# Optimization experiments

Hardware: AMD Instinct MI355X
Metric: run time of the kernel (lower is better)

The kernel has to match this reference:

```python
import jax, jax.numpy as jnp
import numpy as np

N_NODES = 20000
N_EDGES = 160000
N_GRAPHS = 64
IN_DIM = 128
HID = 512
N_CLASSES = 16


def setup_inputs() -> dict:
    key = jax.random.key(0)
    ks = jax.random.split(key, 16)
    x = jax.random.normal(ks[0], (N_NODES, IN_DIM), jnp.float32)
    src = jax.random.randint(ks[1], (N_EDGES,), 0, N_NODES, jnp.int32)
    dst = jax.random.randint(ks[2], (N_EDGES,), 0, N_NODES, jnp.int32)
    graph_ids = jnp.sort(jax.random.randint(ks[3], (N_NODES,), 0, N_GRAPHS, jnp.int32))

    def glorot(k, shape):
        lim = float(np.sqrt(6.0 / (shape[0] + shape[1])))
        return jax.random.uniform(k, shape, jnp.float32, -lim, lim)

    return {
        "x": x, "src": src, "dst": dst, "graph_ids": graph_ids,
        "W1": glorot(ks[4], (IN_DIM, HID)), "b1": jnp.zeros((HID,), jnp.float32),
        "W2": glorot(ks[5], (HID, HID)), "b2": jnp.zeros((HID,), jnp.float32),
        "W3": glorot(ks[6], (HID, HID)), "b3": jnp.zeros((HID,), jnp.float32),
        "Wc1": glorot(ks[7], (HID, HID)), "bc1": jnp.zeros((HID,), jnp.float32),
        "Wc2": glorot(ks[8], (HID, HID)), "bc2": jnp.zeros((HID,), jnp.float32),
        "Wc3": glorot(ks[9], (HID, N_CLASSES)), "bc3": jnp.zeros((N_CLASSES,), jnp.float32),
    }


def _graph_conv(h, W, b, src, dst, dout_isqrt, din_isqrt):
    # DGL GraphConv, norm='both': h' = D_in^{-1/2} A D_out^{-1/2} h W + b
    h = h * dout_isqrt[:, None]          # pre-normalize by sqrt(out-degree)
    h = h @ W                             # project first (cheaper than on edges)
    msg = h[src]                          # gather  [E, out]
    agg = jax.ops.segment_sum(msg, dst, num_segments=N_NODES)  # scatter-add
    return agg * din_isqrt[:, None] + b   # post-normalize by sqrt(in-degree)


def reference(x, src, dst, graph_ids, W1, b1, W2, b2, W3, b3,
              Wc1, bc1, Wc2, bc2, Wc3, bc3):
    ones_e = jnp.ones((N_EDGES,), jnp.float32)
    deg_out = jax.ops.segment_sum(ones_e, src, num_segments=N_NODES)
    deg_in = jax.ops.segment_sum(ones_e, dst, num_segments=N_NODES)
    dout_isqrt = jax.lax.rsqrt(jnp.clip(deg_out, 1.0))
    din_isqrt = jax.lax.rsqrt(jnp.clip(deg_in, 1.0))

    h = jax.nn.relu(_graph_conv(x, W1, b1, src, dst, dout_isqrt, din_isqrt))
    h = jax.nn.relu(_graph_conv(h, W2, b2, src, dst, dout_isqrt, din_isqrt))
    h = jax.nn.relu(_graph_conv(h, W3, b3, src, dst, dout_isqrt, din_isqrt))

    # dgl.mean_nodes: per-graph mean pooling
    sums = jax.ops.segment_sum(h, graph_ids, num_segments=N_GRAPHS)
    counts = jax.ops.segment_sum(jnp.ones((N_NODES,), jnp.float32), graph_ids,
                                 num_segments=N_GRAPHS)
    hg = sums / jnp.clip(counts, 1.0)[:, None]   # [G, HID]

    out = jax.nn.relu(hg @ Wc1 + bc1)
    out = jax.nn.relu(out @ Wc2 + bc2)
    return out @ Wc3 + bc3                       # [G, n_classes]
```

## Files before the change

### kernel.cpp

```cpp
#include <hip/hip_runtime.h>

#define N_NODES 20000
#define N_EDGES 160000
#define N_GRAPHS 64
#define IN_DIM 128
#define HID 512
#define N_CLASSES 16

#define POISON_I ((int)0xAAAAAAAA)

#define DEGCAP 40

typedef unsigned short u16;
typedef short bf16x8 __attribute__((ext_vector_type(8)));
typedef float f32x4 __attribute__((ext_vector_type(4)));

__device__ __forceinline__ u16 bf16_rn(float x) {
  unsigned u = __float_as_uint(x);
  unsigned r = u + 0x7FFFu + ((u >> 16) & 1u);
  return (u16)(r >> 16);
}

__device__ __forceinline__ void addh(float* a, int h) {
  a[0] += __uint_as_float((unsigned)h << 16);
  a[1] += __uint_as_float((unsigned)h & 0xFFFF0000u);
}

#define DEG_BLOCKS ((N_EDGES + 255) / 256)
__global__ void prep(const int* __restrict__ src, const int* __restrict__ dst,
                     int* __restrict__ dout, int* __restrict__ din,
                     int* __restrict__ cursor, int* __restrict__ bucket,
                     const float* __restrict__ W1, const float* __restrict__ W2,
                     const float* __restrict__ W3,
                     u16* __restrict__ w1h, u16* __restrict__ w2h,
                     u16* __restrict__ w3h) {
  if (blockIdx.x < DEG_BLOCKS) {
    const int e = blockIdx.x * 256 + threadIdx.x;
    if (e < N_EDGES) {
      const int s = src[e];
      const int d = dst[e];
      atomicAdd(dout + s, 1);
      atomicAdd(din + d, 1);
      const int pos = atomicAdd(cursor + d, 1) - POISON_I;
      if (pos < DEGCAP) bucket[d * DEGCAP + pos] = s;
    }
  } else {
    const int idx = (blockIdx.x - DEG_BLOCKS) * 256 + threadIdx.x;
    const int n1 = IN_DIM * HID;
    const int n2 = HID * HID;
    const float* W; u16* th; int K, N, j;
    if (idx < n1)             { W = W1; th = w1h; K = IN_DIM; N = HID; j = idx; }
    else if (idx < n1 + n2)   { W = W2; th = w2h; K = HID;    N = HID; j = idx - n1; }
    else if (idx < n1 + 2*n2) { W = W3; th = w3h; K = HID;    N = HID; j = idx - n1 - n2; }
    else return;
    const int k = j / N;
    const int n = j - k * N;
    th[(size_t)n * K + k] = bf16_rn(W[j]);
  }
}

__global__ __launch_bounds__(256) void norms(const int* __restrict__ dout,
                                             const int* __restrict__ din,
                                             float* __restrict__ dosq,
                                             float* __restrict__ disq,
                                             const int* __restrict__ gid,
                                             int* __restrict__ gstart) {
  const int i = blockIdx.x * 256 + threadIdx.x;
  if (i >= N_NODES) return;
  dosq[i] = rsqrtf(fmaxf((float)(dout[i] - POISON_I), 1.0f));
  disq[i] = rsqrtf(fmaxf((float)(din[i] - POISON_I), 1.0f));
  const int g = gid[i];
  const int gp = (i == 0) ? -1 : gid[i - 1];
  for (int k = gp + 1; k <= g; k++) gstart[k] = i;
  if (i == N_NODES - 1) {
    for (int k = g + 1; k <= N_GRAPHS; k++) gstart[k] = N_NODES;
  }
}

__global__ __launch_bounds__(256) void gather_f32(
    const float* __restrict__ x, const int* __restrict__ din,
    const int* __restrict__ bucket, const float* __restrict__ dosq,
    const float* __restrict__ disq, u16* __restrict__ gh) {
  const int node = blockIdx.x * 8 + (threadIdx.x >> 5);
  if (node >= N_NODES) return;
  const int lane4 = (threadIdx.x & 31) * 4;

  int cnt = din[node] - POISON_I;
  if (cnt > DEGCAP) cnt = DEGCAP;
  const int beg = node * DEGCAP;
  const int end = beg + cnt;

  float4 acc = make_float4(0.f, 0.f, 0.f, 0.f);
  int e = beg;
  for (; e + 4 <= end; e += 4) {
    const int s0 = bucket[e], s1 = bucket[e + 1], s2 = bucket[e + 2], s3 = bucket[e + 3];
    const float d0 = dosq[s0], d1 = dosq[s1], d2 = dosq[s2], d3 = dosq[s3];
    const float4 v0 = *(const float4*)(x + (size_t)s0 * IN_DIM + lane4);
    const float4 v1 = *(const float4*)(x + (size_t)s1 * IN_DIM + lane4);
    const float4 v2 = *(const float4*)(x + (size_t)s2 * IN_DIM + lane4);
    const float4 v3 = *(const float4*)(x + (size_t)s3 * IN_DIM + lane4);
    acc.x += d0 * v0.x + d1 * v1.x + d2 * v2.x + d3 * v3.x;
    acc.y += d0 * v0.y + d1 * v1.y + d2 * v2.y + d3 * v3.y;
    acc.z += d0 * v0.z + d1 * v1.z + d2 * v2.z + d3 * v3.z;
    acc.w += d0 * v0.w + d1 * v1.w + d2 * v2.w + d3 * v3.w;
  }
  for (; e < end; e++) {
    const int s0 = bucket[e];
    const float d0 = dosq[s0];
    const float4 v0 = *(const float4*)(x + (size_t)s0 * IN_DIM + lane4);
    acc.x += d0 * v0.x; acc.y += d0 * v0.y; acc.z += d0 * v0.z; acc.w += d0 * v0.w;
  }
  const float di = disq[node];
  ushort4 vh;
  vh.x = bf16_rn(acc.x * di);
  vh.y = bf16_rn(acc.y * di);
  vh.z = bf16_rn(acc.z * di);
  vh.w = bf16_rn(acc.w * di);
  *(ushort4*)(gh + (size_t)node * IN_DIM + lane4) = vh;
}

__global__ __launch_bounds__(256) void gather_hi(
    const u16* __restrict__ hin, const int* __restrict__ din,
    const int* __restrict__ bucket, const float* __restrict__ disq,
    u16* __restrict__ gh) {
  const int node = blockIdx.x * 4 + (threadIdx.x >> 6);
  if (node >= N_NODES) return;
  const int c8 = (threadIdx.x & 63) * 8;
  const u16* base = hin + c8;

  int cnt = din[node] - POISON_I;
  if (cnt > DEGCAP) cnt = DEGCAP;
  const int beg = node * DEGCAP;
  const int end = beg + cnt;

  float acc[8] = {};
  int e = beg;
  for (; e + 8 <= end; e += 8) {
    int s[8];
#pragma unroll
    for (int q = 0; q < 8; q++) s[q] = bucket[e + q];
    int4 h[8];
#pragma unroll
    for (int q = 0; q < 8; q++) h[q] = *(const int4*)(base + (size_t)s[q] * HID);
#pragma unroll
    for (int q = 0; q < 8; q++) {
      addh(acc + 0, h[q].x); addh(acc + 2, h[q].y);
      addh(acc + 4, h[q].z); addh(acc + 6, h[q].w);
    }
  }
  for (; e + 4 <= end; e += 4) {
    const int s0 = bucket[e], s1 = bucket[e + 1], s2 = bucket[e + 2], s3 = bucket[e + 3];
    const int4 h0 = *(const int4*)(base + (size_t)s0 * HID);
    const int4 h1 = *(const int4*)(base + (size_t)s1 * HID);
    const int4 h2 = *(const int4*)(base + (size_t)s2 * HID);
    const int4 h3 = *(const int4*)(base + (size_t)s3 * HID);
    addh(acc + 0, h0.x); addh(acc + 2, h0.y); addh(acc + 4, h0.z); addh(acc + 6, h0.w);
    addh(acc + 0, h1.x); addh(acc + 2, h1.y); addh(acc + 4, h1.z); addh(acc + 6, h1.w);
    addh(acc + 0, h2.x); addh(acc + 2, h2.y); addh(acc + 4, h2.z); addh(acc + 6, h2.w);
    addh(acc + 0, h3.x); addh(acc + 2, h3.y); addh(acc + 4, h3.z); addh(acc + 6, h3.w);
  }
  for (; e < end; e++) {
    const int4 h0 = *(const int4*)(base + (size_t)bucket[e] * HID);
    addh(acc + 0, h0.x); addh(acc + 2, h0.y); addh(acc + 4, h0.z); addh(acc + 6, h0.w);
  }

  const float di = disq[node];
  int4 hi;
  int* hp = (int*)&hi;
#pragma unroll
  for (int i = 0; i < 4; i++) {
    const u16 h0 = bf16_rn(acc[2 * i] * di);
    const u16 h1 = bf16_rn(acc[2 * i + 1] * di);
    hp[i] = (int)h0 | ((int)h1 << 16);
  }
  *(int4*)(gh + (size_t)node * HID + c8) = hi;
}

#define GBK 32
#define LROW 40
template <int POOL>
__global__ __launch_bounds__(256) void gemm_mfma(
    const u16* __restrict__ Ah, int lda,
    const u16* __restrict__ Bh,
    const float* __restrict__ bias, const float* __restrict__ dosq,
    u16* __restrict__ Cb,
    const int* __restrict__ gid, float* __restrict__ hgp,
    int M, int K) {
  __shared__ u16 sAh[128 * LROW];
  __shared__ u16 sBh[128 * LROW];

  const int n = blockIdx.x;
  const int r = (n & 7) + (n >> 5) * 8;
  const int c = (n >> 3) & 3;
  const int row0 = r * 128;
  const int col0 = c * 128;
  if (row0 >= M) return;

  const int t = threadIdx.x;
  const int lane = t & 63;
  const int wav  = t >> 6;
  const int wr = (wav >> 1) * 64;
  const int wc = (wav & 1) * 64;
  const int fm = lane & 15;
  const int fq = lane >> 4;

  const int r0 = t >> 2;
  const int u0 = t & 3;

  f32x4 acc[4][4] = {};

  for (int k0 = 0; k0 < K; k0 += GBK) {
    __syncthreads();
    int4 va[2], vc[2];
#pragma unroll
    for (int rep = 0; rep < 2; rep++) {
      const int row = r0 + rep * 64;
      const int arow = row0 + row;
      const bool ok = arow < M;
      const size_t aoff = (size_t)(ok ? arow : 0) * lda + k0 + u0 * 8;
      va[rep] = ok ? *(const int4*)(Ah + aoff) : make_int4(0, 0, 0, 0);
      const size_t boff = (size_t)(col0 + row) * K + k0 + u0 * 8;
      vc[rep] = *(const int4*)(Bh + boff);
    }
#pragma unroll
    for (int rep = 0; rep < 2; rep++) {
      const int ldso = (r0 + rep * 64) * LROW + u0 * 8;
      *(int4*)(sAh + ldso) = va[rep];
      *(int4*)(sBh + ldso) = vc[rep];
    }
    __syncthreads();

    bf16x8 fah[4], fbh[4];
#pragma unroll
    for (int i = 0; i < 4; i++) {
      const int ar = (wr + i * 16 + fm) * LROW + fq * 8;
      fah[i] = *(const bf16x8*)(sAh + ar);
      const int br = (wc + i * 16 + fm) * LROW + fq * 8;
      fbh[i] = *(const bf16x8*)(sBh + br);
    }
#pragma unroll
    for (int j = 0; j < 4; j++)
#pragma unroll
      for (int i = 0; i < 4; i++)
        acc[i][j] = __builtin_amdgcn_mfma_f32_16x16x32_bf16(fah[i], fbh[j], acc[i][j], 0, 0, 0);
  }

  if (POOL == 0) {
#pragma unroll
    for (int i = 0; i < 4; i++) {
#pragma unroll
      for (int rr = 0; rr < 4; rr++) {
        const int grow = row0 + wr + i * 16 + fq * 4 + rr;
        if (grow < M) {
          const float dsc = dosq[grow];
#pragma unroll
          for (int j = 0; j < 4; j++) {
            const int gcol = col0 + wc + j * 16 + fm;
            const float v = fmaxf(acc[i][j][rr] + bias[gcol], 0.0f) * dsc;
            Cb[(size_t)grow * HID + gcol] = bf16_rn(v);
          }
        }
      }
    }
  } else {
    __syncthreads();
    float* pool = (float*)sAh;
    const int g0 = gid[row0];
    const int rl = (row0 + 127 < M) ? row0 + 127 : M - 1;
    const int gspan = gid[rl] - g0 + 1;
    if (gspan <= 8) {
      for (int i = t; i < gspan * 128; i += 256) pool[i] = 0.f;
      __syncthreads();
#pragma unroll
      for (int j = 0; j < 4; j++) {
        const int lcol = wc + j * 16 + fm;
        const float bv = bias[col0 + lcol];
        float run = 0.f;
        int cur = -1;
#pragma unroll
        for (int i = 0; i < 4; i++)
#pragma unroll
          for (int rr = 0; rr < 4; rr++) {
            const int grow = row0 + wr + i * 16 + fq * 4 + rr;
            if (grow < M) {
              const int sg = gid[grow] - g0;
              const float v = fmaxf(acc[i][j][rr] + bv, 0.0f);
              if (sg != cur) {
                if (cur >= 0) atomicAdd(pool + cur * 128 + lcol, run);
                run = 0.f;
                cur = sg;
              }
              run += v;
            }
          }
        if (cur >= 0) atomicAdd(pool + cur * 128 + lcol, run);
      }
      __syncthreads();
      for (int i = t; i < gspan * 128; i += 256)
        atomicAdd(hgp + (size_t)(g0 + (i >> 7)) * HID + col0 + (i & 127), pool[i]);
    } else {
#pragma unroll
      for (int j = 0; j < 4; j++) {
        const int lcol = wc + j * 16 + fm;
        const float bv = bias[col0 + lcol];
        float run = 0.f;
        int cur = -1;
#pragma unroll
        for (int i = 0; i < 4; i++)
#pragma unroll
          for (int rr = 0; rr < 4; rr++) {
            const int grow = row0 + wr + i * 16 + fq * 4 + rr;
            if (grow < M) {
              const int sg = gid[grow];
              const float v = fmaxf(acc[i][j][rr] + bv, 0.0f);
              if (sg != cur) {
                if (cur >= 0) atomicAdd(hgp + (size_t)cur * HID + col0 + lcol, run);
                run = 0.f;
                cur = sg;
              }
              run += v;
            }
          }
        if (cur >= 0) atomicAdd(hgp + (size_t)cur * HID + col0 + lcol, run);
      }
    }
  }
}

__global__ __launch_bounds__(1024) void mlp_fused(
    const float* __restrict__ hgp, const int* __restrict__ gstart,
    const float* __restrict__ Wc1, const float* __restrict__ bc1,
    const float* __restrict__ Wc2, const float* __restrict__ bc2,
    const float* __restrict__ Wc3, const float* __restrict__ bc3,
    float* __restrict__ out) {
  __shared__ float sA[HID];
  __shared__ float sB[HID];
  __shared__ float4 red4[8][128];
  float* red = (float*)red4;

  const int g = blockIdx.x;
  const int t = threadIdx.x;
  const int cg = t & 127;
  const int sl = t >> 7;

  if (t < HID) {
    const float inv = 1.0f / fmaxf((float)(gstart[g + 1] - gstart[g]), 1.0f);
    sA[t] = hgp[(size_t)g * HID + t] * inv;
  }
  __syncthreads();

  {
    float4 a = make_float4(0.f, 0.f, 0.f, 0.f);
    const int kb = sl * 64;
#pragma unroll 8
    for (int k = kb; k < kb + 64; k++) {
      const float s = sA[k];
      const float4 w = *(const float4*)(Wc1 + (size_t)k * HID + cg * 4);
      a.x += s * w.x; a.y += s * w.y; a.z += s * w.z; a.w += s * w.w;
    }
    red4[sl][cg] = a;
  }
  __syncthreads();
  if (sl == 0) {
    float4 a = red4[0][cg];
#pragma unroll
    for (int s = 1; s < 8; s++) {
      const float4 b = red4[s][cg];
      a.x += b.x; a.y += b.y; a.z += b.z; a.w += b.w;
    }
    const float4 b = *(const float4*)(bc1 + cg * 4);
    sB[cg * 4 + 0] = fmaxf(a.x + b.x, 0.f);
    sB[cg * 4 + 1] = fmaxf(a.y + b.y, 0.f);
    sB[cg * 4 + 2] = fmaxf(a.z + b.z, 0.f);
    sB[cg * 4 + 3] = fmaxf(a.w + b.w, 0.f);
  }
  __syncthreads();

  {
    float4 a = make_float4(0.f, 0.f, 0.f, 0.f);
    const int kb = sl * 64;
#pragma unroll 8
    for (int k = kb; k < kb + 64; k++) {
      const float s = sB[k];
      const float4 w = *(const float4*)(Wc2 + (size_t)k * HID + cg * 4);
      a.x += s * w.x; a.y += s * w.y; a.z += s * w.z; a.w += s * w.w;
    }
    red4[sl][cg] = a;
  }
  __syncthreads();
  if (sl == 0) {
    float4 a = red4[0][cg];
#pragma unroll
    for (int s = 1; s < 8; s++) {
      const float4 b = red4[s][cg];
      a.x += b.x; a.y += b.y; a.z += b.z; a.w += b.w;
    }
    const float4 b = *(const float4*)(bc2 + cg * 4);
    sA[cg * 4 + 0] = fmaxf(a.x + b.x, 0.f);
    sA[cg * 4 + 1] = fmaxf(a.y + b.y, 0.f);
    sA[cg * 4 + 2] = fmaxf(a.z + b.z, 0.f);
    sA[cg * 4 + 3] = fmaxf(a.w + b.w, 0.f);
  }
  __syncthreads();

  {
    const int col = t & 15;
    const int s3 = t >> 4;
    float a = 0.f;
#pragma unroll 8
    for (int k = s3; k < HID; k += 64) a += sA[k] * Wc3[(size_t)k * N_CLASSES + col];
    red[t] = a;
  }
  __syncthreads();
#pragma unroll
  for (int off = 512; off >= 16; off >>= 1) {
    if (t < off) red[t] += red[t + off];
    __syncthreads();
  }
  if (t < 16) out[(size_t)g * N_CLASSES + t] = red[t] + bc3[t];
}

extern "C" void kernel_launch(void* const* d_in, const int* in_sizes, int n_in,
                              void* d_out, int out_size, void* d_ws, size_t ws_size,
                              hipStream_t stream) {
  const float* x   = (const float*)d_in[0];
  const int*   src = (const int*)d_in[1];
  const int*   dst = (const int*)d_in[2];
  const int*   gid = (const int*)d_in[3];
  const float* W1  = (const float*)d_in[4];  const float* b1  = (const float*)d_in[5];
  const float* W2  = (const float*)d_in[6];  const float* b2  = (const float*)d_in[7];
  const float* W3  = (const float*)d_in[8];  const float* b3  = (const float*)d_in[9];
  const float* Wc1 = (const float*)d_in[10]; const float* bc1 = (const float*)d_in[11];
  const float* Wc2 = (const float*)d_in[12]; const float* bc2 = (const float*)d_in[13];
  const float* Wc3 = (const float*)d_in[14]; const float* bc3 = (const float*)d_in[15];
  float* out = (float*)d_out;

  char* p = (char*)d_ws;
  u16* gA = (u16*)p;                  p += (size_t)N_NODES * HID * 2;
  u16* hB = (u16*)p;                  p += (size_t)N_NODES * HID * 2;
  u16* w1h = (u16*)p;                 p += (size_t)HID * IN_DIM * 2;
  u16* w2h = (u16*)p;                 p += (size_t)HID * HID * 2;
  u16* w3h = (u16*)p;                 p += (size_t)HID * HID * 2;
  float* dosq = (float*)p;            p += N_NODES * 4;
  float* disq = (float*)p;            p += N_NODES * 4;
  float* hgp = (float*)p;             p += (size_t)N_GRAPHS * HID * 4;
  int* deg_out_i = (int*)p;           p += N_NODES * 4;
  int* deg_in_i  = (int*)p;           p += N_NODES * 4;
  int* cursor    = (int*)p;           p += N_NODES * 4;
  int* gstart    = (int*)p;           p += (N_GRAPHS + 1) * 4;
  int* bucket    = (int*)p;           p += (size_t)N_NODES * DEGCAP * 4;

  const int wprep_blocks = (IN_DIM * HID + 2 * HID * HID + 255) / 256;
  prep<<<DEG_BLOCKS + wprep_blocks, 256, 0, stream>>>(
      src, dst, deg_out_i, deg_in_i, cursor, bucket, W1, W2, W3, w1h, w2h, w3h);
  norms<<<(N_NODES + 255) / 256, 256, 0, stream>>>(deg_out_i, deg_in_i, dosq, disq, gid, gstart);

  const int ggrid = 640;
  const int gat_blocks = (N_NODES + 3) / 4;

  gather_f32<<<(N_NODES + 7) / 8, 256, 0, stream>>>(x, deg_in_i, bucket, dosq, disq, gA);
  gemm_mfma<0><<<ggrid, 256, 0, stream>>>(gA, IN_DIM, w1h, b1, dosq, hB, gid, hgp, N_NODES, IN_DIM);

  gather_hi<<<gat_blocks, 256, 0, stream>>>(hB, deg_in_i, bucket, disq, gA);
  gemm_mfma<0><<<ggrid, 256, 0, stream>>>(gA, HID, w2h, b2, dosq, hB, gid, hgp, N_NODES, HID);

  gather_hi<<<gat_blocks, 256, 0, stream>>>(hB, deg_in_i, bucket, disq, gA);
  gemm_mfma<1><<<ggrid, 256, 0, stream>>>(gA, HID, w3h, b3, dosq, nullptr, gid, hgp, N_NODES, HID);

  mlp_fused<<<N_GRAPHS, 1024, 0, stream>>>(hgp, gstart, Wc1, bc1, Wc2, bc2, Wc3, bc3, out);
}
```

Baseline: 262.3 us.

## Double-buffer GEMM tiles, tile weight transpose, reuse cursor as in-degree

Double-buffers the MFMA GEMM's shared-memory tiles, prefetching the next K slice into registers while computing the current one, which removes one barrier per iteration. Converts the weight transpose into a 64x64 shared-memory tiled transpose for coalesced writes. Drops the separate in-degree atomic and reuses the bucket cursor count. Unrolls the first-layer gather to 8 edges for more loads in flight. Costs extra LDS and registers, which may reduce occupancy.

```diff
diff --git a/kernel.cpp b/kernel.cpp
--- a/kernel.cpp
+++ b/kernel.cpp
@@ -27,35 +27,44 @@
 }
 
 #define DEG_BLOCKS ((N_EDGES + 255) / 256)
+#define TT_BLOCKS 144
 __global__ void prep(const int* __restrict__ src, const int* __restrict__ dst,
-                     int* __restrict__ dout, int* __restrict__ din,
+                     int* __restrict__ dout,
                      int* __restrict__ cursor, int* __restrict__ bucket,
                      const float* __restrict__ W1, const float* __restrict__ W2,
                      const float* __restrict__ W3,
                      u16* __restrict__ w1h, u16* __restrict__ w2h,
                      u16* __restrict__ w3h) {
+  __shared__ u16 tile[64][65];
   if (blockIdx.x < DEG_BLOCKS) {
     const int e = blockIdx.x * 256 + threadIdx.x;
     if (e < N_EDGES) {
       const int s = src[e];
       const int d = dst[e];
       atomicAdd(dout + s, 1);
-      atomicAdd(din + d, 1);
       const int pos = atomicAdd(cursor + d, 1) - POISON_I;
       if (pos < DEGCAP) bucket[d * DEGCAP + pos] = s;
     }
-  } else {
-    const int idx = (blockIdx.x - DEG_BLOCKS) * 256 + threadIdx.x;
-    const int n1 = IN_DIM * HID;
-    const int n2 = HID * HID;
-    const float* W; u16* th; int K, N, j;
-    if (idx < n1)             { W = W1; th = w1h; K = IN_DIM; N = HID; j = idx; }
-    else if (idx < n1 + n2)   { W = W2; th = w2h; K = HID;    N = HID; j = idx - n1; }
-    else if (idx < n1 + 2*n2) { W = W3; th = w3h; K = HID;    N = HID; j = idx - n1 - n2; }
-    else return;
-    const int k = j / N;
-    const int n = j - k * N;
-    th[(size_t)n * K + k] = bf16_rn(W[j]);
+    return;
+  }
+  const int b = blockIdx.x - DEG_BLOCKS;
+  const float* W; u16* th; int K, k0, n0;
+  if (b < 16)      { W = W1; th = w1h; K = IN_DIM; k0 = (b & 1) * 64;        n0 = (b >> 1) * 64; }
+  else if (b < 80) { W = W2; th = w2h; K = HID;    k0 = ((b - 16) & 7) * 64; n0 = ((b - 16) >> 3) * 64; }
+  else             { W = W3; th = w3h; K = HID;    k0 = ((b - 80) & 7) * 64; n0 = ((b - 80) >> 3) * 64; }
+  const int t = threadIdx.x;
+  const int tn = t & 63;
+  const int tk4 = t >> 6;
+#pragma unroll
+  for (int pass = 0; pass < 16; pass++) {
+    const int k = pass * 4 + tk4;
+    tile[tn][k] = bf16_rn(W[(size_t)(k0 + k) * HID + n0 + tn]);
+  }
+  __syncthreads();
+#pragma unroll
+  for (int pass = 0; pass < 16; pass++) {
+    const int n = pass * 4 + tk4;
+    th[(size_t)(n0 + n) * K + k0 + tn] = tile[n][tn];
   }
 }
 
@@ -92,17 +101,22 @@
 
   float4 acc = make_float4(0.f, 0.f, 0.f, 0.f);
   int e = beg;
-  for (; e + 4 <= end; e += 4) {
-    const int s0 = bucket[e], s1 = bucket[e + 1], s2 = bucket[e + 2], s3 = bucket[e + 3];
-    const float d0 = dosq[s0], d1 = dosq[s1], d2 = dosq[s2], d3 = dosq[s3];
-    const float4 v0 = *(const float4*)(x + (size_t)s0 * IN_DIM + lane4);
-    const float4 v1 = *(const float4*)(x + (size_t)s1 * IN_DIM + lane4);
-    const float4 v2 = *(const float4*)(x + (size_t)s2 * IN_DIM + lane4);
-    const float4 v3 = *(const float4*)(x + (size_t)s3 * IN_DIM + lane4);
-    acc.x += d0 * v0.x + d1 * v1.x + d2 * v2.x + d3 * v3.x;
-    acc.y += d0 * v0.y + d1 * v1.y + d2 * v2.y + d3 * v3.y;
-    acc.z += d0 * v0.z + d1 * v1.z + d2 * v2.z + d3 * v3.z;
-    acc.w += d0 * v0.w + d1 * v1.w + d2 * v2.w + d3 * v3.w;
+  for (; e + 8 <= end; e += 8) {
+    int s[8];
+#pragma unroll
+    for (int q = 0; q < 8; q++) s[q] = bucket[e + q];
+    float4 v[8];
+    float dd[8];
+#pragma unroll
+    for (int q = 0; q < 8; q++) {
+      dd[q] = dosq[s[q]];
+      v[q] = *(const float4*)(x + (size_t)s[q] * IN_DIM + lane4);
+    }
+#pragma unroll
+    for (int q = 0; q < 8; q++) {
+      acc.x += dd[q] * v[q].x; acc.y += dd[q] * v[q].y;
+      acc.z += dd[q] * v[q].z; acc.w += dd[q] * v[q].w;
+    }
   }
   for (; e < end; e++) {
     const int s0 = bucket[e];
@@ -186,8 +200,8 @@
     u16* __restrict__ Cb,
     const int* __restrict__ gid, float* __restrict__ hgp,
     int M, int K) {
-  __shared__ u16 sAh[128 * LROW];
-  __shared__ u16 sBh[128 * LROW];
+  __shared__ u16 sAh[2][128 * LROW];
+  __shared__ u16 sBh[2][128 * LROW];
 
   const int n = blockIdx.x;
   const int r = (n & 7) + (n >> 5) * 8;
@@ -207,42 +221,61 @@
   const int r0 = t >> 2;
   const int u0 = t & 3;
 
+  const int arow0 = row0 + r0;
+  const int arow1 = row0 + r0 + 64;
+  const size_t aoff0 = (size_t)((arow0 < M) ? arow0 : 0) * lda + u0 * 8;
+  const size_t aoff1 = (size_t)((arow1 < M) ? arow1 : 0) * lda + u0 * 8;
+  const size_t boff0 = (size_t)(col0 + r0) * K + u0 * 8;
+  const size_t boff1 = (size_t)(col0 + r0 + 64) * K + u0 * 8;
+  const int ldso0 = r0 * LROW + u0 * 8;
+  const int ldso1 = (r0 + 64) * LROW + u0 * 8;
+
   f32x4 acc[4][4] = {};
 
+  {
+    const int4 va0 = *(const int4*)(Ah + aoff0);
+    const int4 va1 = *(const int4*)(Ah + aoff1);
+    const int4 vb0 = *(const int4*)(Bh + boff0);
+    const int4 vb1 = *(const int4*)(Bh + boff1);
+    *(int4*)(sAh[0] + ldso0) = va0;
+    *(int4*)(sAh[0] + ldso1) = va1;
+    *(int4*)(sBh[0] + ldso0) = vb0;
+    *(int4*)(sBh[0] + ldso1) = vb1;
+  }
+  __syncthreads();
+
+  int cur = 0;
   for (int k0 = 0; k0 < K; k0 += GBK) {
-    __syncthreads();
-    int4 va[2], vc[2];
-#pragma unroll
-    for (int rep = 0; rep < 2; rep++) {
-      const int row = r0 + rep * 64;
-      const int arow = row0 + row;
-      const bool ok = arow < M;
-      const size_t aoff = (size_t)(ok ? arow : 0) * lda + k0 + u0 * 8;
-      va[rep] = ok ? *(const int4*)(Ah + aoff) : make_int4(0, 0, 0, 0);
-      const size_t boff = (size_t)(col0 + row) * K + k0 + u0 * 8;
-      vc[rep] = *(const int4*)(Bh + boff);
-    }
-#pragma unroll
-    for (int rep = 0; rep < 2; rep++) {
-      const int ldso = (r0 + rep * 64) * LROW + u0 * 8;
-      *(int4*)(sAh + ldso) = va[rep];
-      *(int4*)(sBh + ldso) = vc[rep];
-    }
-    __syncthreads();
+    const bool has_next = (k0 + GBK) < K;
+    int4 va0, va1, vb0, vb1;
+    if (has_next) {
+      const int kn = k0 + GBK;
+      va0 = *(const int4*)(Ah + aoff0 + kn);
+      va1 = *(const int4*)(Ah + aoff1 + kn);
+      vb0 = *(const int4*)(Bh + boff0 + kn);
+      vb1 = *(const int4*)(Bh + boff1 + kn);
+    }
 
     bf16x8 fah[4], fbh[4];
 #pragma unroll
     for (int i = 0; i < 4; i++) {
-      const int ar = (wr + i * 16 + fm) * LROW + fq * 8;
-      fah[i] = *(const bf16x8*)(sAh + ar);
-      const int br = (wc + i * 16 + fm) * LROW + fq * 8;
-      fbh[i] = *(const bf16x8*)(sBh + br);
+      fah[i] = *(const bf16x8*)(sAh[cur] + (wr + i * 16 + fm) * LROW + fq * 8);
+      fbh[i] = *(const bf16x8*)(sBh[cur] + (wc + i * 16 + fm) * LROW + fq * 8);
     }
 #pragma unroll
     for (int j = 0; j < 4; j++)
 #pragma unroll
       for (int i = 0; i < 4; i++)
         acc[i][j] = __builtin_amdgcn_mfma_f32_16x16x32_bf16(fah[i], fbh[j], acc[i][j], 0, 0, 0);
+
+    if (has_next) {
+      *(int4*)(sAh[cur ^ 1] + ldso0) = va0;
+      *(int4*)(sAh[cur ^ 1] + ldso1) = va1;
+      *(int4*)(sBh[cur ^ 1] + ldso0) = vb0;
+      *(int4*)(sBh[cur ^ 1] + ldso1) = vb1;
+    }
+    __syncthreads();
+    cur ^= 1;
   }
 
   if (POOL == 0) {
@@ -263,7 +296,6 @@
       }
     }
   } else {
-    __syncthreads();
     float* pool = (float*)sAh;
     const int g0 = gid[row0];
     const int rl = (row0 + 127 < M) ? row0 + 127 : M - 1;
@@ -276,7 +308,7 @@
         const int lcol = wc + j * 16 + fm;
         const float bv = bias[col0 + lcol];
         float run = 0.f;
-        int cur = -1;
+        int cur2 = -1;
 #pragma unroll
         for (int i = 0; i < 4; i++)
 #pragma unroll
@@ -285,15 +317,15 @@
             if (grow < M) {
               const int sg = gid[grow] - g0;
               const float v = fmaxf(acc[i][j][rr] + bv, 0.0f);
-              if (sg != cur) {
-                if (cur >= 0) atomicAdd(pool + cur * 128 + lcol, run);
+              if (sg != cur2) {
+                if (cur2 >= 0) atomicAdd(pool + cur2 * 128 + lcol, run);
                 run = 0.f;
-                cur = sg;
+                cur2 = sg;
               }
               run += v;
             }
           }
-        if (cur >= 0) atomicAdd(pool + cur * 128 + lcol, run);
+        if (cur2 >= 0) atomicAdd(pool + cur2 * 128 + lcol, run);
       }
       __syncthreads();
       for (int i = t; i < gspan * 128; i += 256)
@@ -304,7 +336,7 @@
         const int lcol = wc + j * 16 + fm;
         const float bv = bias[col0 + lcol];
         float run = 0.f;
-        int cur = -1;
+        int cur2 = -1;
 #pragma unroll
         for (int i = 0; i < 4; i++)
 #pragma unroll
@@ -313,15 +345,15 @@
             if (grow < M) {
               const int sg = gid[grow];
               const float v = fmaxf(acc[i][j][rr] + bv, 0.0f);
-              if (sg != cur) {
-                if (cur >= 0) atomicAdd(hgp + (size_t)cur * HID + col0 + lcol, run);
+              if (sg != cur2) {
+                if (cur2 >= 0) atomicAdd(hgp + (size_t)cur2 * HID + col0 + lcol, run);
                 run = 0.f;
-                cur = sg;
+                cur2 = sg;
               }
               run += v;
             }
           }
-        if (cur >= 0) atomicAdd(hgp + (size_t)cur * HID + col0 + lcol, run);
+        if (cur2 >= 0) atomicAdd(hgp + (size_t)cur2 * HID + col0 + lcol, run);
       }
     }
   }
@@ -445,26 +477,24 @@
   float* disq = (float*)p;            p += N_NODES * 4;
   float* hgp = (float*)p;             p += (size_t)N_GRAPHS * HID * 4;
   int* deg_out_i = (int*)p;           p += N_NODES * 4;
-  int* deg_in_i  = (int*)p;           p += N_NODES * 4;
   int* cursor    = (int*)p;           p += N_NODES * 4;
   int* gstart    = (int*)p;           p += (N_GRAPHS + 1) * 4;
   int* bucket    = (int*)p;           p += (size_t)N_NODES * DEGCAP * 4;
 
-  const int wprep_blocks = (IN_DIM * HID + 2 * HID * HID + 255) / 256;
-  prep<<<DEG_BLOCKS + wprep_blocks, 256, 0, stream>>>(
-      src, dst, deg_out_i, deg_in_i, cursor, bucket, W1, W2, W3, w1h, w2h, w3h);
-  norms<<<(N_NODES + 255) / 256, 256, 0, stream>>>(deg_out_i, deg_in_i, dosq, disq, gid, gstart);
+  prep<<<DEG_BLOCKS + TT_BLOCKS, 256, 0, stream>>>(
+      src, dst, deg_out_i, cursor, bucket, W1, W2, W3, w1h, w2h, w3h);
+  norms<<<(N_NODES + 255) / 256, 256, 0, stream>>>(deg_out_i, cursor, dosq, disq, gid, gstart);
 
   const int ggrid = 640;
   const int gat_blocks = (N_NODES + 3) / 4;
 
-  gather_f32<<<(N_NODES + 7) / 8, 256, 0, stream>>>(x, deg_in_i, bucket, dosq, disq, gA);
+  gather_f32<<<(N_NODES + 7) / 8, 256, 0, stream>>>(x, cursor, bucket, dosq, disq, gA);
   gemm_mfma<0><<<ggrid, 256, 0, stream>>>(gA, IN_DIM, w1h, b1, dosq, hB, gid, hgp, N_NODES, IN_DIM);
 
-  gather_hi<<<gat_blocks, 256, 0, stream>>>(hB, deg_in_i, bucket, disq, gA);
+  gather_hi<<<gat_blocks, 256, 0, stream>>>(hB, cursor, bucket, disq, gA);
   gemm_mfma<0><<<ggrid, 256, 0, stream>>>(gA, HID, w2h, b2, dosq, hB, gid, hgp, N_NODES, HID);
 
-  gather_hi<<<gat_blocks, 256, 0, stream>>>(hB, deg_in_i, bucket, disq, gA);
+  gather_hi<<<gat_blocks, 256, 0, stream>>>(hB, cursor, bucket, disq, gA);
   gemm_mfma<1><<<ggrid, 256, 0, stream>>>(gA, HID, w3h, b3, dosq, nullptr, gid, hgp, N_NODES, HID);
 
   mlp_fused<<<N_GRAPHS, 1024, 0, stream>>>(hgp, gstart, Wc1, bc1, Wc2, bc2, Wc3, bc3, out);
```

New measurement: 252.8 us. 1.04x faster.
